# Kernel optimization log

Measured on AMD Instinct MI355X. Metric: run time of the kernel, lower is better.

Reference implementation:

```python
import jax, jax.numpy as jnp
import numpy as np

D = 128
H = 4
DK = D // H


def _spmm(row, col, val, x, n):
    # sparse.mm(adj, x) with adj in COO form: out[row] += val * x[col]
    return jax.ops.segment_sum(val[:, None] * x[col], row, num_segments=n)


def _arrg(h, a1_w, a1_b, a2_w, a2_b):
    return jax.nn.leaky_relu(h @ a1_w + a1_b, negative_slope=0.01) @ a2_w + a2_b


def _cross_attn(x, q_x, q_w, k_w, v_w):
    n, d = x.shape
    m = q_x.shape[0]
    q = (q_x @ q_w).reshape(m, H, DK).transpose(1, 0, 2)   # [H, Q, dk]
    k = (x @ k_w).reshape(n, H, DK).transpose(1, 0, 2)     # [H, N, dk]
    v = (q_x @ v_w).reshape(m, H, DK).transpose(1, 0, 2)   # [H, Q, dk]
    s = jnp.einsum('hnd,hqd->hnq', k, q) / jnp.sqrt(jnp.float32(DK))
    w = jax.nn.softmax(s, axis=-1)                          # softmax over queries
    out = jnp.einsum('hnq,hqd->hnd', w, v).transpose(1, 0, 2).reshape(n, d)
    return out + x


def setup_inputs() -> dict:
    key = jax.random.key(0)
    ks = iter(jax.random.split(key, 64))
    nrm = lambda shape, s=0.05: jax.random.normal(next(ks), shape, jnp.float32) * s
    inp = {}
    inp['trans_w'] = nrm((1, D)); inp['trans_b'] = nrm((D,))
    inp['g_w'] = nrm((D, D));     inp['g_b'] = nrm((D,))
    inp['qg_w'] = nrm((D, D));    inp['qg_b'] = nrm((D,))
    inp['q_w'] = nrm((D, D)); inp['k_w'] = nrm((D, D)); inp['v_w'] = nrm((D, D))
    inp['a1_w'] = nrm((D, 2 * D)); inp['a1_b'] = nrm((2 * D,))
    inp['a2_w'] = nrm((2 * D, D)); inp['a2_b'] = nrm((D,))
    inp['x0'] = jax.random.normal(next(ks), (25000,), jnp.float32)
    inp['q0'] = jax.random.normal(next(ks), (100,), jnp.float32)
    for i in (1, 2, 3):
        inp[f'xin{i}'] = jax.random.normal(next(ks), (25000,), jnp.float32)
        inp[f'qin{i}'] = jax.random.normal(next(ks), (100,), jnp.float32)
    n_sizes = {1: 50000, 2: 75000, 3: 100000}
    q_sizes = {1: 200, 2: 300, 3: 400}
    for i in (1, 2, 3):
        e = 16 * n_sizes[i]
        inp[f'aval{i}'] = jax.random.uniform(next(ks), (e,), jnp.float32)
        inp[f'arow{i}'] = jax.random.randint(next(ks), (e,), 0, n_sizes[i], jnp.int64)
        inp[f'acol{i}'] = jax.random.randint(next(ks), (e,), 0, n_sizes[i], jnp.int64)
        qe = 16 * q_sizes[i]
        inp[f'qval{i}'] = jax.random.uniform(next(ks), (qe,), jnp.float32)
        inp[f'qrow{i}'] = jax.random.randint(next(ks), (qe,), 0, q_sizes[i], jnp.int64)
        inp[f'qcol{i}'] = jax.random.randint(next(ks), (qe,), 0, q_sizes[i], jnp.int64)
    return inp


def reference(trans_w, trans_b, g_w, g_b, qg_w, qg_b, q_w, k_w, v_w,
              a1_w, a1_b, a2_w, a2_b,
              x0, q0, xin1, xin2, xin3, qin1, qin2, qin3,
              aval1, aval2, aval3, qval1, qval2, qval3,
              arow1, acol1, arow2, acol2, arow3, acol3,
              qrow1, qcol1, qrow2, qcol2, qrow3, qcol3):
    trans = lambda v: v[:, None] @ trans_w + trans_b
    x = trans(x0)
    qx = trans(q0)
    steps = [
        (xin1, qin1, arow1, acol1, aval1, qrow1, qcol1, qval1, 50000, 200),
        (xin2, qin2, arow2, acol2, aval2, qrow2, qcol2, qval2, 75000, 300),
        (xin3, qin3, arow3, acol3, aval3, qrow3, qcol3, qval3, 100000, 400),
    ]
    for xin, qin, ar, ac, av, qr, qc, qv, n, m in steps:
        x = jnp.concatenate([x, trans(xin)], axis=0)
        qx = jnp.concatenate([qx, trans(qin)], axis=0)
        x = _spmm(ar, ac, av, x @ g_w + g_b, n)
        qx = _spmm(qr, qc, qv, qx @ qg_w + qg_b, m)
        x = _arrg(x, a1_w, a1_b, a2_w, a2_b)
        qx = _arrg(qx, a1_w, a1_b, a2_w, a2_b)
        x = _cross_attn(x, qx, q_w, k_w, v_w)
    return (x, qx)
```

## Files before the change

kernel.cpp:

```cpp
#include <hip/hip_runtime.h>

typedef unsigned short u16;
typedef __attribute__((ext_vector_type(8))) short bf16x8;
typedef __attribute__((ext_vector_type(4))) float f32x4;
typedef __attribute__((ext_vector_type(2))) unsigned u32x2;

__device__ __forceinline__ float b2f(u16 v) {
    return __uint_as_float(((unsigned)v) << 16);
}
__device__ __forceinline__ u16 f2b(float x) {
    unsigned u = __float_as_uint(x);
    unsigned r = u + 0x7FFFu + ((u >> 16) & 1u);
    return (u16)(r >> 16);
}
__device__ __forceinline__ float4 load_bf4(const u16* p) {
    ushort4 q = *(const ushort4*)p;
    float4 f;
    f.x = b2f(q.x); f.y = b2f(q.y); f.z = b2f(q.z); f.w = b2f(q.w);
    return f;
}
__device__ __forceinline__ float4 in4(const void* p, long off, bool bf) {
    if (bf) return load_bf4((const u16*)p + off);
    return *(const float4*)((const float*)p + off);
}
// ... 45 lines not shown
                                 const void* __restrict__ k_w, const void* __restrict__ q_w,
                                 const void* __restrict__ v_w,
                                 u16* __restrict__ Wg, u16* __restrict__ Wqg,
                                 u16* __restrict__ Wa1, u16* __restrict__ Wa2,
                                 u16* __restrict__ Wk, u16* __restrict__ Wq,
                                 u16* __restrict__ Wv, const int* __restrict__ flags) {
    const bool bf = flags[0] != 0;
    int idx = blockIdx.x * blockDim.x + threadIdx.x;
    const void* src; u16* dst; int K, N, loc;
    if (idx < 32768) {
        if (idx < 16384) { src = g_w; dst = Wg; loc = idx; }
        else { src = qg_w; dst = Wqg; loc = idx - 16384; }
        K = 128; N = 128;
    } else if (idx < 65536) { src = a1_w; dst = Wa1; loc = idx - 32768; K = 128; N = 256; }
    else if (idx < 98304)  { src = a2_w; dst = Wa2; loc = idx - 65536; K = 256; N = 128; }
    else if (idx < 147456) {
        if (idx < 114688) { src = k_w; dst = Wk; loc = idx - 98304; }
        else if (idx < 131072) { src = q_w; dst = Wq; loc = idx - 114688; }
        else { src = v_w; dst = Wv; loc = idx - 131072; }
        K = 128; N = 128;
    } else return;
    int j = loc & 7, lane = (loc >> 3) & 63, t = loc >> 9;
    int KC = K >> 5;
    int kc = t % KC, ct = t / KC;
    int k = kc * 32 + (lane >> 4) * 8 + j;
    int nn = ct * 16 + (lane & 15);
    dst[loc] = f2b(in1(src, (long)k * N + nn, bf));
}

template<int KTOT, int NOUT, bool LEAKY, typename AT, typename CT>
__launch_bounds__(256)
__global__ void gemm_mfma_kernel(const AT* __restrict__ A, const u16* __restrict__ Wf,
                                 const void* __restrict__ bias, CT* __restrict__ C,
                                 int n, const int* __restrict__ flags) {
    constexpr int KC = KTOT / 32;
    constexpr int NT = NOUT / 16;
    __shared__ u16 wlds[KTOT * NOUT];
    {
        const int4* srcw = (const int4*)Wf;
        int4* dstw = (int4*)wlds;
        constexpr int NV = KTOT * NOUT * 2 / 16;
#pragma unroll
        for (int i = 0; i < NV / 256; ++i)
            dstw[i * 256 + threadIdx.x] = srcw[i * 256 + threadIdx.x];
    }
    __syncthreads();
    const bool bf = flags[0] != 0;
    const int lane = threadIdx.x & 63;
    const int wave = threadIdx.x >> 6;
    const int quad = lane >> 4, col = lane & 15;
    const int rbase = (blockIdx.x * 4 + wave) * 16;
    if (rbase >= n) return;
    int node = rbase + col; if (node >= n) node = n - 1;
    f32x4 acc[NT];
#pragma unroll
    for (int ct = 0; ct < NT; ++ct) acc[ct] = (f32x4){0.f, 0.f, 0.f, 0.f};
#pragma unroll
    for (int kc = 0; kc < KC; ++kc) {
        bf16x8 af;
        if constexpr (sizeof(AT) == 2) {
            af = *(const bf16x8*)((const u16*)A + (size_t)node * KTOT + kc * 32 + quad * 8);
        } else {
            const float* ap = (const float*)A + (size_t)node * KTOT + kc * 32 + quad * 8;
            float4 a0 = *(const float4*)ap;
            float4 a1 = *(const float4*)(ap + 4);
            af[0] = (short)f2b(a0.x); af[1] = (short)f2b(a0.y);
            af[2] = (short)f2b(a0.z); af[3] = (short)f2b(a0.w);
            af[4] = (short)f2b(a1.x); af[5] = (short)f2b(a1.y);
            af[6] = (short)f2b(a1.z); af[7] = (short)f2b(a1.w);
        }
#pragma unroll
        for (int ct = 0; ct < NT; ++ct) {
            bf16x8 wf = *(const bf16x8*)(wlds + (((ct * KC + kc) * 64 + lane) * 8));
            acc[ct] = __builtin_amdgcn_mfma_f32_16x16x32_bf16(af, wf, acc[ct], 0, 0, 0);
        }
    }
#pragma unroll
    for (int ct = 0; ct < NT; ++ct) {
        int colg = ct * 16 + col;
        float b = bias ? in1(bias, colg, bf) : 0.f;
#pragma unroll
        for (int r = 0; r < 4; ++r) {
            int row = rbase + quad * 4 + r;
            if (row >= n) continue;
            float v = acc[ct][r] + b;
            if (LEAKY) v = v > 0.f ? v : 0.01f * v;
            if constexpr (sizeof(CT) == 2) C[(size_t)row * NOUT + colg] = (CT)f2b(v);
            else                           C[(size_t)row * NOUT + colg] = (CT)v;
        }
    }
}

__launch_bounds__(256)
__global__ void gemm_qv_kernel(const float* __restrict__ A, const u16* __restrict__ Wfq,
                               const u16* __restrict__ Wfv, u16* __restrict__ Qf,
                               u16* __restrict__ Vf, int m, int mt32) {
    __shared__ u16 wldsq[128 * 128];
    __shared__ u16 wldsv[128 * 128];
    {
        const int4* sq = (const int4*)Wfq;
        const int4* sv = (const int4*)Wfv;
        int4* dq = (int4*)wldsq;
        int4* dv = (int4*)wldsv;
#pragma unroll
        for (int i = 0; i < 8; ++i) {
            dq[i * 256 + threadIdx.x] = sq[i * 256 + threadIdx.x];
            dv[i * 256 + threadIdx.x] = sv[i * 256 + threadIdx.x];
        }
    }
    __syncthreads();
    const int mpad = mt32 * 32;
    const int mt16 = mt32 * 2;
    const int lane = threadIdx.x & 63;
    const int wave = threadIdx.x >> 6;
    const int quad = lane >> 4, col = lane & 15;
    const int rbase = (blockIdx.x * 4 + wave) * 16;
    if (rbase >= mpad) return;
    int node = rbase + col; if (node >= m) node = m - 1;
    f32x4 accq[8], accv[8];
#pragma unroll
    for (int ct = 0; ct < 8; ++ct) {
        accq[ct] = (f32x4){0.f, 0.f, 0.f, 0.f};
        accv[ct] = (f32x4){0.f, 0.f, 0.f, 0.f};
    }
#pragma unroll
    for (int kc = 0; kc < 4; ++kc) {
        const float* ap = A + (size_t)node * 128 + kc * 32 + quad * 8;
        float4 a0 = *(const float4*)ap;
        float4 a1 = *(const float4*)(ap + 4);
        bf16x8 af;
        af[0] = (short)f2b(a0.x); af[1] = (short)f2b(a0.y);
        af[2] = (short)f2b(a0.z); af[3] = (short)f2b(a0.w);
        af[4] = (short)f2b(a1.x); af[5] = (short)f2b(a1.y);
        af[6] = (short)f2b(a1.z); af[7] = (short)f2b(a1.w);
#pragma unroll
        for (int ct = 0; ct < 8; ++ct) {
            bf16x8 wq = *(const bf16x8*)(wldsq + (((ct * 4 + kc) * 64 + lane) * 8));
            bf16x8 wv = *(const bf16x8*)(wldsv + (((ct * 4 + kc) * 64 + lane) * 8));
            accq[ct] = __builtin_amdgcn_mfma_f32_16x16x32_bf16(af, wq, accq[ct], 0, 0, 0);
            accv[ct] = __builtin_amdgcn_mfma_f32_16x16x32_bf16(af, wv, accv[ct], 0, 0, 0);
        }
    }
    const float qscale = 0.17677669529663687f * 1.44269504088896340736f;
#pragma unroll
    for (int ct = 0; ct < 8; ++ct) {
        int colg = ct * 16 + col;
        int h = colg >> 5, dim = colg & 31;
#pragma unroll
        for (int r = 0; r < 4; ++r) {
            int row = rbase + quad * 4 + r;
            if (row >= mpad) continue;
            bool pad = row >= m;
            float vq = pad ? 0.f : accq[ct][r] * qscale;
            float vv = pad ? 0.f : accv[ct][r];
            {
                size_t idx = ((((size_t)h * mt16 + (row >> 4)) * 64)
                              + ((dim >> 3) << 4) + (row & 15)) * 8 + (dim & 7);
                Qf[idx] = f2b(vq);
            }
            {
                size_t idx = (((((size_t)h * mt32 + (row >> 5)) * 2 + (dim >> 4)) * 64)
                              + (((row >> 3) & 3) << 4) + (dim & 15)) * 8 + (row & 7);
                Vf[idx] = f2b(vv);
            }
        }
    }
}

#define RSH 8
#define NBC_MAX 512
#define EPB 4096
#define BSTRIDE 6144

__global__ void ginit_kernel(int* __restrict__ p, int nbc) {
    int i = blockIdx.x * blockDim.x + threadIdx.x;
    if (i < nbc) p[i] = i * BSTRIDE;
}

__launch_bounds__(256)
__global__ void qbuild_kernel(const void* __restrict__ rows, const void* __restrict__ colsin,
                              const void* __restrict__ valsin, int e, int nrows,
                              int2* __restrict__ pack1, int* __restrict__ rowptr,
                              int* __restrict__ rowend, const int* __restrict__ flags) {
    __shared__ int hist[512], cur[512], sc[512];
    const bool bf = flags[0] != 0;
    const bool i64 = flags[1] != 0;
    const int tid = threadIdx.x;
    for (int i = tid; i < 512; i += 256) hist[i] = 0;
    __syncthreads();
    for (int i = tid; i < e; i += 256)
        atomicAdd(&hist[inIdx(rows, i, i64)], 1);
    __syncthreads();
    int v0 = hist[tid], v1 = hist[tid + 256];
    sc[tid] = v0; sc[tid + 256] = v1;
    __syncthreads();
    for (int off = 1; off < 512; off <<= 1) {
        int a = (tid >= off) ? sc[tid - off] : 0;
        int b = sc[tid + 256 - off];
        __syncthreads();
        sc[tid] += a;
        sc[tid + 256] += b;
        __syncthreads();
    }
    {
        int x = sc[tid] - v0;
        cur[tid] = x;
        if (tid < nrows) { rowptr[tid] = x; rowend[tid] = x + v0; }
        int x1 = sc[tid + 256] - v1;
        cur[tid + 256] = x1;
        if (tid + 256 < nrows) { rowptr[tid + 256] = x1; rowend[tid + 256] = x1 + v1; }
    }
    __syncthreads();
    for (int i = tid; i < e; i += 256) {
        int r = inIdx(rows, i, i64);
        int p = atomicAdd(&cur[r], 1);
        pack1[p] = (int2){inIdx(colsin, i, i64), __float_as_int(in1(valsin, i, bf))};
    }
}

__launch_bounds__(256)
__global__ void psort_kernel(const void* __restrict__ rows, const void* __restrict__ colsin,
                             const void* __restrict__ valsin, int e,
                             int* __restrict__ gcur, int2* __restrict__ pack0,
                             int nbc, const int* __restrict__ flags) {
    __shared__ int hist[NBC_MAX];
    __shared__ int scan[NBC_MAX];
    __shared__ int base[NBC_MAX];
    __shared__ int cur[NBC_MAX];
    __shared__ int2 stage[EPB];
    __shared__ u16 binof[EPB];
    const bool bf = flags[0] != 0;
    const bool i64 = flags[1] != 0;
    const int tid = threadIdx.x;
    const long s0 = (long)blockIdx.x * EPB;
    int cnt_e = e - (int)s0; if (cnt_e > EPB) cnt_e = EPB;

    for (int i = tid; i < NBC_MAX; i += 256) hist[i] = 0;
    __syncthreads();
    for (int j = tid; j < cnt_e; j += 256)
        atomicAdd(&hist[inIdx(rows, s0 + j, i64) >> RSH], 1);
    __syncthreads();
    for (int i = tid; i < NBC_MAX; i += 256) scan[i] = hist[i];
    __syncthreads();
    for (int off = 1; off < NBC_MAX; off <<= 1) {
        int a = (tid >= off) ? scan[tid - off] : 0;
        int c = scan[tid + 256 - off];
        __syncthreads();
        scan[tid] += a;
        scan[tid + 256] += c;
        __syncthreads();
    }
    for (int i = tid; i < nbc; i += 256) {
        int h = hist[i];
        cur[i] = scan[i] - h;
        base[i] = h ? atomicAdd(&gcur[i], h) : 0;
    }
    __syncthreads();
    for (int j = tid; j < cnt_e; j += 256) {
        int r = inIdx(rows, s0 + j, i64);
        int bin = r >> RSH;
        int p = atomicAdd(&cur[bin], 1);
        int2 pk;
        pk.x = ((r & ((1 << RSH) - 1)) << 20) | inIdx(colsin, s0 + j, i64);
        pk.y = __float_as_int(in1(valsin, s0 + j, bf));
        stage[p] = pk;
        binof[p] = (u16)bin;
    }
    __syncthreads();
    for (int j = tid; j < cnt_e; j += 256) {
        int bin = binof[j];
        int st = scan[bin] - hist[bin];
        pack0[base[bin] + (j - st)] = stage[j];
    }
}

__launch_bounds__(256)
__global__ void breorder256_kernel(const int2* __restrict__ pack0, const int* __restrict__ bend,
                                   int2* __restrict__ pack1,
                                   int* __restrict__ rowptr, int* __restrict__ rowend, int n) {
    __shared__ int hist[256], scan[256], cur[256];
    const int b = blockIdx.x;
    const int s = b * BSTRIDE, e = bend[b];
    const int tid = threadIdx.x;
    hist[tid] = 0;
    __syncthreads();
    for (int i = s + tid; i < e; i += 256)
        atomicAdd(&hist[(unsigned)pack0[i].x >> 20], 1);
    __syncthreads();
    scan[tid] = hist[tid];
    __syncthreads();
    for (int off = 1; off < 256; off <<= 1) {
        int a = (tid >= off) ? scan[tid - off] : 0;
        __syncthreads();
        scan[tid] += a;
        __syncthreads();
    }
    int st = s + scan[tid] - hist[tid];
    cur[tid] = st;
    int rg = (b << RSH) + tid;
    if (rg < n) { rowptr[rg] = st; rowend[rg] = st + hist[tid]; }
    __syncthreads();
    for (int i = s + tid; i < e; i += 256) {
        int2 pk = pack0[i];
        int rl = (unsigned)pk.x >> 20;
        int p = atomicAdd(&cur[rl], 1);
        pack1[p] = (int2){pk.x & 0xFFFFF, pk.y};
    }
}

__device__ __forceinline__ void bffma8(float v, uint4 h, float* a) {
    a[0] += v * __uint_as_float(h.x << 16);
    a[1] += v * __uint_as_float(h.x & 0xFFFF0000u);
    a[2] += v * __uint_as_float(h.y << 16);
    a[3] += v * __uint_as_float(h.y & 0xFFFF0000u);
    a[4] += v * __uint_as_float(h.z << 16);
    a[5] += v * __uint_as_float(h.z & 0xFFFF0000u);
    a[6] += v * __uint_as_float(h.w << 16);
    a[7] += v * __uint_as_float(h.w & 0xFFFF0000u);
// ... 8 lines not shown
    const int s16 = lane >> 4;
    const int l16 = lane & 15;
    int s = rowptr[r], e = rowend[r];
    float a[8] = {0.f, 0.f, 0.f, 0.f, 0.f, 0.f, 0.f, 0.f};
    int i = s + s16;
    for (; i + 12 < e; i += 16) {
        int2 p0 = pack[i], p1 = pack[i + 4], p2 = pack[i + 8], p3 = pack[i + 12];
        uint4 h0 = *(const uint4*)(H + (size_t)p0.x * 128 + l16 * 8);
        uint4 h1 = *(const uint4*)(H + (size_t)p1.x * 128 + l16 * 8);
        uint4 h2 = *(const uint4*)(H + (size_t)p2.x * 128 + l16 * 8);
        uint4 h3 = *(const uint4*)(H + (size_t)p3.x * 128 + l16 * 8);
        bffma8(__int_as_float(p0.y), h0, a);
        bffma8(__int_as_float(p1.y), h1, a);
        bffma8(__int_as_float(p2.y), h2, a);
        bffma8(__int_as_float(p3.y), h3, a);
    }
    for (; i < e; i += 4) {
        int2 p0 = pack[i];
        uint4 h0 = *(const uint4*)(H + (size_t)p0.x * 128 + l16 * 8);
        bffma8(__int_as_float(p0.y), h0, a);
    }
#pragma unroll
    for (int k = 0; k < 8; ++k) {
        a[k] += __shfl_xor(a[k], 16, 64);
        a[k] += __shfl_xor(a[k], 32, 64);
    }
    if (s16 == 0) {
        uint4 o;
        o.x = (unsigned)f2b(a[0]) | ((unsigned)f2b(a[1]) << 16);
        o.y = (unsigned)f2b(a[2]) | ((unsigned)f2b(a[3]) << 16);
        o.z = (unsigned)f2b(a[4]) | ((unsigned)f2b(a[5]) << 16);
        o.w = (unsigned)f2b(a[6]) | ((unsigned)f2b(a[7]) << 16);
        *(uint4*)(out + (size_t)r * 128 + l16 * 8) = o;
    }
}

__launch_bounds__(256)
__global__ void attn_mfma_kernel(const u16* __restrict__ Kb, const u16* __restrict__ Qf,
                                 const u16* __restrict__ Vf, float* __restrict__ X,
                                 int n, int m, int mt32, int pad) {
    __shared__ __align__(128) u16 Pbuf_all[4 * 1024];
    const int h = blockIdx.y;
    const int wave = threadIdx.x >> 6;
    const int lane = threadIdx.x & 63;
    const int nb = (blockIdx.x * 4 + wave) * 32;
    if (nb >= n) return;
    const int quad = lane >> 4, col = lane & 15;
    int node0 = nb + col;      if (node0 >= n) node0 = n - 1;
    int node1 = nb + 16 + col; if (node1 >= n) node1 = n - 1;
    bf16x8 kf0 = *(const bf16x8*)(Kb + (size_t)node0 * 128 + h * 32 + quad * 8);
    bf16x8 kf1 = *(const bf16x8*)(Kb + (size_t)node1 * 128 + h * 32 + quad * 8);
    f32x4 O00 = {0.f, 0.f, 0.f, 0.f}, O01 = {0.f, 0.f, 0.f, 0.f};
    f32x4 O10 = {0.f, 0.f, 0.f, 0.f}, O11 = {0.f, 0.f, 0.f, 0.f};
    const f32x4 zero = {0.f, 0.f, 0.f, 0.f};
    float Lp0[4] = {0.f, 0.f, 0.f, 0.f};
    float Lp1[4] = {0.f, 0.f, 0.f, 0.f};
    u16* Pw0 = Pbuf_all + wave * 1024;
    u16* Pw1 = Pw0 + 512;
    uint2* pw0[2]; uint2* pw1[2];
    pw0[0] = (uint2*)(Pw0 + col * 16 + quad * 4);
    pw0[1] = (uint2*)(Pw0 + 256 + col * 16 + quad * 4);
    pw1[0] = (uint2*)(Pw1 + col * 16 + quad * 4);
    pw1[1] = (uint2*)(Pw1 + 256 + col * 16 + quad * 4);
    const unsigned paddr0 = (unsigned)(uintptr_t)Pw0 + (unsigned)(quad * 256 + col * 8);
    const unsigned paddr1 = (unsigned)(uintptr_t)Pw1 + (unsigned)(quad * 256 + col * 8);
    const u16* Qbase = Qf + (size_t)h * (mt32 * 2) * 512;
// ... 134 lines not shown
    };
    int*   flags = (int*)alloc(256);
    const int NMAX = 100000;
    const int NBINS = (NMAX + 255) >> RSH;
    float* X   = (float*)alloc((size_t)NMAX * 128 * 4);
    u16*   T1b = (u16*)  alloc((size_t)NMAX * 128 * 2);
    u16*   Xs  = (u16*)  alloc((size_t)NMAX * 128 * 2);
    u16*   T2  = (u16*)  alloc((size_t)NMAX * 256 * 2);
    float* QX  = (float*)alloc((size_t)400 * 128 * 4);
    u16*   QT1b= (u16*)  alloc((size_t)400 * 128 * 2);
    u16*   QXs = (u16*)  alloc((size_t)400 * 128 * 2);
    u16*   QT2 = (u16*)  alloc((size_t)400 * 256 * 2);
    u16*   Qfrag = (u16*)alloc((size_t)4 * 13 * 1024 * 2);
    u16*   Vfrag = (u16*)alloc((size_t)4 * 13 * 1024 * 2);
    u16* Wg  = (u16*)alloc((size_t)128 * 128 * 2);
    u16* Wqg = (u16*)alloc((size_t)128 * 128 * 2);
    u16* Wa1 = (u16*)alloc((size_t)128 * 256 * 2);
    u16* Wa2 = (u16*)alloc((size_t)256 * 128 * 2);
    u16* Wk  = (u16*)alloc((size_t)128 * 128 * 2);
    u16* Wq  = (u16*)alloc((size_t)128 * 128 * 2);
    u16* Wv  = (u16*)alloc((size_t)128 * 128 * 2);
    int2*  csr_pack = (int2*)alloc((size_t)(NBINS + 1) * BSTRIDE * 8);
    int*   bktcur = (int*)alloc((size_t)NBC_MAX * 4);
    int*   rowptr = (int*)alloc((size_t)NMAX * 4);
    int*   rowend = (int*)alloc((size_t)NMAX * 4);
    int2*  pack0  = (int2*)T2;

    sniff_kernel<<<1, 64, 0, stream>>>((const u16*)x0, (const int*)d_in[iarow[0]], flags);

    wprep_all_kernel<<<(147456 + 255) / 256, 256, 0, stream>>>(
        g_w, qg_w, a1_w, a2_w, k_w, q_w, v_w,
        Wg, Wqg, Wa1, Wa2, Wk, Wq, Wv, flags);

    auto launch_trans2 = [&](const void* vx, float* outx, int rowsx,
                             const void* vq, float* outq, int rowsq) {
        int tot = (rowsx + rowsq) * 32;
        trans2_kernel<<<(tot + 255) / 256, 256, 0, stream>>>(vx, outx, rowsx,
                                                             vq, outq, rowsq,
                                                             trans_w, trans_b, flags);
    };
    auto build_spmm = [&](const void* rows, const void* colsidx, const void* vals, int e,
                          int nrows, const u16* H, u16* OUT) {
        if (nrows <= 512) {
            qbuild_kernel<<<1, 256, 0, stream>>>(rows, colsidx, vals, e, nrows,
                                                 csr_pack, rowptr, rowend, flags);
        } else {
            int nbc = (nrows + 255) >> RSH;
            ginit_kernel<<<(nbc + 255) / 256, 256, 0, stream>>>(bktcur, nbc);
            psort_kernel<<<(e + EPB - 1) / EPB, 256, 0, stream>>>(rows, colsidx, vals, e,
                                                                  bktcur, pack0, nbc, flags);
            breorder256_kernel<<<nbc, 256, 0, stream>>>(pack0, bktcur, csr_pack,
                                                        rowptr, rowend, nrows);
        }
        spmm_kernel<<<(nrows + 3) / 4, 256, 0, stream>>>(H, rowptr, rowend, csr_pack,
                                                         OUT, nrows);
    };

    int nprev = in_sizes[13];
    int mprev = in_sizes[14];
    launch_trans2(x0, X, nprev, q0, QX, mprev);

    const int ns[3] = {50000, 75000, 100000};
    const int ms[3] = {200, 300, 400};
    for (int s = 0; s < 3; ++s) {
        const int n = ns[s], m = ms[s];
        const int e  = in_sizes[iaval[s]];
        const int qe = in_sizes[iqval[s]];
        launch_trans2(d_in[ixin[s]], X + (size_t)nprev * 128, n - nprev,
                      d_in[iqin[s]], QX + (size_t)mprev * 128, m - mprev);
        const int gb  = (n + 63) / 64;
        const int gqb = (m + 63) / 64;
        gemm_mfma_kernel<128, 128, false, float, u16><<<gb, 256, 0, stream>>>(X, Wg, g_b, T1b, n, flags);
        build_spmm(d_in[iarow[s]], d_in[iacol[s]], d_in[iaval[s]], e, n, T1b, Xs);
        gemm_mfma_kernel<128, 128, false, float, u16><<<gqb, 256, 0, stream>>>(QX, Wqg, qg_b, QT1b, m, flags);
        build_spmm(d_in[iqrow[s]], d_in[iqcol[s]], d_in[iqval[s]], qe, m, QT1b, QXs);
        gemm_mfma_kernel<128, 256, true, u16, u16><<<gb, 256, 0, stream>>>(Xs, Wa1, a1_b, T2, n, flags);
        gemm_mfma_kernel<256, 128, false, u16, float><<<gb, 256, 0, stream>>>(T2, Wa2, a2_b, X, n, flags);
        gemm_mfma_kernel<128, 256, true, u16, u16><<<gqb, 256, 0, stream>>>(QXs, Wa1, a1_b, QT2, m, flags);
        gemm_mfma_kernel<256, 128, false, u16, float><<<gqb, 256, 0, stream>>>(QT2, Wa2, a2_b, QX, m, flags);
        const int mt32 = (m + 31) / 32;
        const int pad = mt32 * 32 - m;
        gemm_mfma_kernel<128, 128, false, float, u16><<<gb, 256, 0, stream>>>(X, Wk, nullptr, T1b, n, flags);
        gemm_qv_kernel<<<(mt32 * 32 + 63) / 64, 256, 0, stream>>>(QX, Wq, Wv, Qfrag, Vfrag, m, mt32);
        attn_mfma_kernel<<<dim3((n + 127) / 128, 4), 256, 0, stream>>>(T1b, Qfrag, Vfrag, X, n, m, mt32, pad);
        nprev = n;
        mprev = m;
    }

    const int n4t = (100000 + 400) * 128 / 4;
    out_writer_kernel<<<(n4t + 255) / 256, 256, 0, stream>>>(X, QX, d_out, flags);
}
```

Measured before the change: 1.144 ms.

## Fuse query-branch pipeline into one kernel and fold trans into the g-GEMM

The whole small query-side step (trans, qg GEMM, CSR build, SpMM, two MLP GEMMs, Q/V projection) is merged into a single 1024-thread block kernel that reloads weights into shared memory between phases. The per-step trans kernel for new x rows is folded into the A-load of the first GEMM, and the bucket cursor reset moves into breorder. These changes cut kernel launch count and avoid materialising the new trans rows. The cost is that the query work now runs serially on one CU with many block-wide barriers, and csr_pack is shared between the query and node paths, which relies on stream ordering.

```diff
diff --git a/kernel.cpp b/kernel.cpp
--- a/kernel.cpp
+++ b/kernel.cpp
@@ -101,7 +101,9 @@
 __launch_bounds__(256)
 __global__ void gemm_mfma_kernel(const AT* __restrict__ A, const u16* __restrict__ Wf,
                                  const void* __restrict__ bias, CT* __restrict__ C,
-                                 int n, const int* __restrict__ flags) {
+                                 int n, const int* __restrict__ flags,
+                                 const void* __restrict__ vap, int nprevP,
+                                 const void* __restrict__ twp, const void* __restrict__ tbp) {
     constexpr int KC = KTOT / 32;
     constexpr int NT = NOUT / 16;
     __shared__ u16 wlds[KTOT * NOUT];
@@ -130,13 +132,24 @@
         if constexpr (sizeof(AT) == 2) {
             af = *(const bf16x8*)((const u16*)A + (size_t)node * KTOT + kc * 32 + quad * 8);
         } else {
-            const float* ap = (const float*)A + (size_t)node * KTOT + kc * 32 + quad * 8;
-            float4 a0 = *(const float4*)ap;
-            float4 a1 = *(const float4*)(ap + 4);
-            af[0] = (short)f2b(a0.x); af[1] = (short)f2b(a0.y);
-            af[2] = (short)f2b(a0.z); af[3] = (short)f2b(a0.w);
-            af[4] = (short)f2b(a1.x); af[5] = (short)f2b(a1.y);
-            af[6] = (short)f2b(a1.z); af[7] = (short)f2b(a1.w);
+            int c0 = kc * 32 + quad * 8;
+            if (vap && node >= nprevP) {
+                float v = in1(vap, node - nprevP, bf);
+                float4 w0 = in4(twp, c0, bf), w1 = in4(twp, c0 + 4, bf);
+                float4 b0 = in4(tbp, c0, bf), b1 = in4(tbp, c0 + 4, bf);
+                af[0] = (short)f2b(v * w0.x + b0.x); af[1] = (short)f2b(v * w0.y + b0.y);
+                af[2] = (short)f2b(v * w0.z + b0.z); af[3] = (short)f2b(v * w0.w + b0.w);
+                af[4] = (short)f2b(v * w1.x + b1.x); af[5] = (short)f2b(v * w1.y + b1.y);
+                af[6] = (short)f2b(v * w1.z + b1.z); af[7] = (short)f2b(v * w1.w + b1.w);
+            } else {
+                const float* ap = (const float*)A + (size_t)node * KTOT + c0;
+                float4 a0 = *(const float4*)ap;
+                float4 a1 = *(const float4*)(ap + 4);
+                af[0] = (short)f2b(a0.x); af[1] = (short)f2b(a0.y);
+                af[2] = (short)f2b(a0.z); af[3] = (short)f2b(a0.w);
+                af[4] = (short)f2b(a1.x); af[5] = (short)f2b(a1.y);
+                af[6] = (short)f2b(a1.z); af[7] = (short)f2b(a1.w);
+            }
         }
 #pragma unroll
         for (int ct = 0; ct < NT; ++ct) {
@@ -160,82 +173,6 @@
     }
 }
 
-__launch_bounds__(256)
-__global__ void gemm_qv_kernel(const float* __restrict__ A, const u16* __restrict__ Wfq,
-                               const u16* __restrict__ Wfv, u16* __restrict__ Qf,
-                               u16* __restrict__ Vf, int m, int mt32) {
-    __shared__ u16 wldsq[128 * 128];
-    __shared__ u16 wldsv[128 * 128];
-    {
-        const int4* sq = (const int4*)Wfq;
-        const int4* sv = (const int4*)Wfv;
-        int4* dq = (int4*)wldsq;
-        int4* dv = (int4*)wldsv;
-#pragma unroll
-        for (int i = 0; i < 8; ++i) {
-            dq[i * 256 + threadIdx.x] = sq[i * 256 + threadIdx.x];
-            dv[i * 256 + threadIdx.x] = sv[i * 256 + threadIdx.x];
-        }
-    }
-    __syncthreads();
-    const int mpad = mt32 * 32;
-    const int mt16 = mt32 * 2;
-    const int lane = threadIdx.x & 63;
-    const int wave = threadIdx.x >> 6;
-    const int quad = lane >> 4, col = lane & 15;
-    const int rbase = (blockIdx.x * 4 + wave) * 16;
-    if (rbase >= mpad) return;
-    int node = rbase + col; if (node >= m) node = m - 1;
-    f32x4 accq[8], accv[8];
-#pragma unroll
-    for (int ct = 0; ct < 8; ++ct) {
-        accq[ct] = (f32x4){0.f, 0.f, 0.f, 0.f};
-        accv[ct] = (f32x4){0.f, 0.f, 0.f, 0.f};
-    }
-#pragma unroll
-    for (int kc = 0; kc < 4; ++kc) {
-        const float* ap = A + (size_t)node * 128 + kc * 32 + quad * 8;
-        float4 a0 = *(const float4*)ap;
-        float4 a1 = *(const float4*)(ap + 4);
-        bf16x8 af;
-        af[0] = (short)f2b(a0.x); af[1] = (short)f2b(a0.y);
-        af[2] = (short)f2b(a0.z); af[3] = (short)f2b(a0.w);
-        af[4] = (short)f2b(a1.x); af[5] = (short)f2b(a1.y);
-        af[6] = (short)f2b(a1.z); af[7] = (short)f2b(a1.w);
-#pragma unroll
-        for (int ct = 0; ct < 8; ++ct) {
-            bf16x8 wq = *(const bf16x8*)(wldsq + (((ct * 4 + kc) * 64 + lane) * 8));
-            bf16x8 wv = *(const bf16x8*)(wldsv + (((ct * 4 + kc) * 64 + lane) * 8));
-            accq[ct] = __builtin_amdgcn_mfma_f32_16x16x32_bf16(af, wq, accq[ct], 0, 0, 0);
-            accv[ct] = __builtin_amdgcn_mfma_f32_16x16x32_bf16(af, wv, accv[ct], 0, 0, 0);
-        }
-    }
-    const float qscale = 0.17677669529663687f * 1.44269504088896340736f;
-#pragma unroll
-    for (int ct = 0; ct < 8; ++ct) {
-        int colg = ct * 16 + col;
-        int h = colg >> 5, dim = colg & 31;
-#pragma unroll
-        for (int r = 0; r < 4; ++r) {
-            int row = rbase + quad * 4 + r;
-            if (row >= mpad) continue;
-            bool pad = row >= m;
-            float vq = pad ? 0.f : accq[ct][r] * qscale;
-            float vv = pad ? 0.f : accv[ct][r];
-            {
-                size_t idx = ((((size_t)h * mt16 + (row >> 4)) * 64)
-                              + ((dim >> 3) << 4) + (row & 15)) * 8 + (dim & 7);
-                Qf[idx] = f2b(vq);
-            }
-            {
-                size_t idx = (((((size_t)h * mt32 + (row >> 5)) * 2 + (dim >> 4)) * 64)
-                              + (((row >> 3) & 3) << 4) + (dim & 15)) * 8 + (row & 7);
-                Vf[idx] = f2b(vv);
-            }
-        }
-    }
-}
-
 #define RSH 8
 #define NBC_MAX 512
 #define EPB 4096
@@ -244,47 +181,6 @@
 __global__ void ginit_kernel(int* __restrict__ p, int nbc) {
     int i = blockIdx.x * blockDim.x + threadIdx.x;
     if (i < nbc) p[i] = i * BSTRIDE;
-}
-
-__launch_bounds__(256)
-__global__ void qbuild_kernel(const void* __restrict__ rows, const void* __restrict__ colsin,
-                              const void* __restrict__ valsin, int e, int nrows,
-                              int2* __restrict__ pack1, int* __restrict__ rowptr,
-                              int* __restrict__ rowend, const int* __restrict__ flags) {
-    __shared__ int hist[512], cur[512], sc[512];
-    const bool bf = flags[0] != 0;
-    const bool i64 = flags[1] != 0;
-    const int tid = threadIdx.x;
-    for (int i = tid; i < 512; i += 256) hist[i] = 0;
-    __syncthreads();
-    for (int i = tid; i < e; i += 256)
-        atomicAdd(&hist[inIdx(rows, i, i64)], 1);
-    __syncthreads();
-    int v0 = hist[tid], v1 = hist[tid + 256];
-    sc[tid] = v0; sc[tid + 256] = v1;
-    __syncthreads();
-    for (int off = 1; off < 512; off <<= 1) {
-        int a = (tid >= off) ? sc[tid - off] : 0;
-        int b = sc[tid + 256 - off];
-        __syncthreads();
-        sc[tid] += a;
-        sc[tid + 256] += b;
-        __syncthreads();
-    }
-    {
-        int x = sc[tid] - v0;
-        cur[tid] = x;
-        if (tid < nrows) { rowptr[tid] = x; rowend[tid] = x + v0; }
-        int x1 = sc[tid + 256] - v1;
-        cur[tid + 256] = x1;
-        if (tid + 256 < nrows) { rowptr[tid + 256] = x1; rowend[tid + 256] = x1 + v1; }
-    }
-    __syncthreads();
-    for (int i = tid; i < e; i += 256) {
-        int r = inIdx(rows, i, i64);
-        int p = atomicAdd(&cur[r], 1);
-        pack1[p] = (int2){inIdx(colsin, i, i64), __float_as_int(in1(valsin, i, bf))};
-    }
 }
 
 __launch_bounds__(256)
@@ -344,7 +240,7 @@
 }
 
 __launch_bounds__(256)
-__global__ void breorder256_kernel(const int2* __restrict__ pack0, const int* __restrict__ bend,
+__global__ void breorder256_kernel(const int2* __restrict__ pack0, int* __restrict__ bend,
                                    int2* __restrict__ pack1,
                                    int* __restrict__ rowptr, int* __restrict__ rowend, int n) {
     __shared__ int hist[256], scan[256], cur[256];
@@ -353,6 +249,7 @@
     const int tid = threadIdx.x;
     hist[tid] = 0;
     __syncthreads();
+    if (tid == 0) bend[b] = b * BSTRIDE;
     for (int i = s + tid; i < e; i += 256)
         atomicAdd(&hist[(unsigned)pack0[i].x >> 20], 1);
     __syncthreads();
@@ -427,6 +324,282 @@
         o.z = (unsigned)f2b(a[4]) | ((unsigned)f2b(a[5]) << 16);
         o.w = (unsigned)f2b(a[6]) | ((unsigned)f2b(a[7]) << 16);
         *(uint4*)(out + (size_t)r * 128 + l16 * 8) = o;
+    }
+}
+
+__launch_bounds__(1024)
+__global__ void qstep_kernel(float* __restrict__ QX, const void* __restrict__ qin, int mprev,
+                             const u16* __restrict__ Wqg, const void* __restrict__ qg_b,
+                             const u16* __restrict__ Wa1, const void* __restrict__ a1_b,
+                             const u16* __restrict__ Wa2, const void* __restrict__ a2_b,
+                             const u16* __restrict__ Wq, const u16* __restrict__ Wv,
+                             const void* __restrict__ qrow, const void* __restrict__ qcol,
+                             const void* __restrict__ qval, int qe,
+                             u16* __restrict__ QT1b, u16* __restrict__ QXs,
+                             u16* __restrict__ QT2,
+                             int2* __restrict__ qpack,
+                             u16* __restrict__ Qf, u16* __restrict__ Vf,
+                             int m, int mt32,
+                             const void* __restrict__ tw, const void* __restrict__ tb,
+                             const int* __restrict__ flags) {
+    __shared__ u16 wbuf[32768];
+    __shared__ int hist[512], cur[512], sc[512];
+    const bool bf = flags[0] != 0;
+    const bool i64 = flags[1] != 0;
+    const int tid = threadIdx.x;
+    const int lane = tid & 63;
+    const int wv = tid >> 6;
+    const int quad = lane >> 4, col = lane & 15;
+    const int ntile = (m + 15) >> 4;
+    const f32x4 zero4 = {0.f, 0.f, 0.f, 0.f};
+
+    {
+        const int4* s4 = (const int4*)Wqg;
+        int4* d4 = (int4*)wbuf;
+        for (int i = tid; i < 2048; i += 1024) d4[i] = s4[i];
+    }
+    __syncthreads();
+    for (int t = wv; t < ntile; t += 16) {
+        int rbase = t * 16;
+        int node = rbase + col; if (node >= m) node = m - 1;
+        f32x4 acc[8];
+#pragma unroll
+        for (int ct = 0; ct < 8; ++ct) acc[ct] = zero4;
+#pragma unroll
+        for (int kc = 0; kc < 4; ++kc) {
+            bf16x8 af;
+            int c0 = kc * 32 + quad * 8;
+            if (node >= mprev) {
+                float v = in1(qin, node - mprev, bf);
+                float4 w0 = in4(tw, c0, bf), w1 = in4(tw, c0 + 4, bf);
+                float4 b0 = in4(tb, c0, bf), b1 = in4(tb, c0 + 4, bf);
+                af[0] = (short)f2b(v * w0.x + b0.x); af[1] = (short)f2b(v * w0.y + b0.y);
+                af[2] = (short)f2b(v * w0.z + b0.z); af[3] = (short)f2b(v * w0.w + b0.w);
+                af[4] = (short)f2b(v * w1.x + b1.x); af[5] = (short)f2b(v * w1.y + b1.y);
+                af[6] = (short)f2b(v * w1.z + b1.z); af[7] = (short)f2b(v * w1.w + b1.w);
+            } else {
+                const float* ap = QX + (size_t)node * 128 + c0;
+                float4 a0 = *(const float4*)ap, a1 = *(const float4*)(ap + 4);
+                af[0] = (short)f2b(a0.x); af[1] = (short)f2b(a0.y);
+                af[2] = (short)f2b(a0.z); af[3] = (short)f2b(a0.w);
+                af[4] = (short)f2b(a1.x); af[5] = (short)f2b(a1.y);
+                af[6] = (short)f2b(a1.z); af[7] = (short)f2b(a1.w);
+            }
+#pragma unroll
+            for (int ct = 0; ct < 8; ++ct) {
+                bf16x8 wf = *(const bf16x8*)(wbuf + (((ct * 4 + kc) * 64 + lane) * 8));
+                acc[ct] = __builtin_amdgcn_mfma_f32_16x16x32_bf16(af, wf, acc[ct], 0, 0, 0);
+            }
+        }
+#pragma unroll
+        for (int ct = 0; ct < 8; ++ct) {
+            int colg = ct * 16 + col;
+            float b = in1(qg_b, colg, bf);
+#pragma unroll
+            for (int r = 0; r < 4; ++r) {
+                int row = rbase + quad * 4 + r;
+                if (row < m) QT1b[(size_t)row * 128 + colg] = f2b(acc[ct][r] + b);
+            }
+        }
+    }
+    for (int i = tid; i < 512; i += 1024) hist[i] = 0;
+    __syncthreads();
+    for (int i = tid; i < qe; i += 1024)
+        atomicAdd(&hist[inIdx(qrow, i, i64)], 1);
+    __syncthreads();
+    int v0 = (tid < 512) ? hist[tid] : 0;
+    if (tid < 512) sc[tid] = v0;
+    __syncthreads();
+    for (int off = 1; off < 512; off <<= 1) {
+        int a = (tid < 512 && tid >= off) ? sc[tid - off] : 0;
+        __syncthreads();
+        if (tid < 512) sc[tid] += a;
+        __syncthreads();
+    }
+    if (tid < 512) {
+        int x = sc[tid] - v0;
+        hist[tid] = x;
+        cur[tid] = x;
+    }
+    __syncthreads();
+    for (int i = tid; i < qe; i += 1024) {
+        int r = inIdx(qrow, i, i64);
+        int p = atomicAdd(&cur[r], 1);
+        qpack[p] = (int2){inIdx(qcol, i, i64), __float_as_int(in1(qval, i, bf))};
+    }
+    __syncthreads();
+    __threadfence();
+    {
+        const int s16 = lane >> 4, l16 = lane & 15;
+        for (int r = wv; r < m; r += 16) {
+            int s = hist[r], e = sc[r];
+            float a[8] = {0.f, 0.f, 0.f, 0.f, 0.f, 0.f, 0.f, 0.f};
+            int i = s + s16;
+            for (; i + 12 < e; i += 16) {
+                int2 p0 = qpack[i], p1 = qpack[i + 4], p2 = qpack[i + 8], p3 = qpack[i + 12];
+                uint4 h0 = *(const uint4*)(QT1b + (size_t)p0.x * 128 + l16 * 8);
+                uint4 h1 = *(const uint4*)(QT1b + (size_t)p1.x * 128 + l16 * 8);
+                uint4 h2 = *(const uint4*)(QT1b + (size_t)p2.x * 128 + l16 * 8);
+                uint4 h3 = *(const uint4*)(QT1b + (size_t)p3.x * 128 + l16 * 8);
+                bffma8(__int_as_float(p0.y), h0, a);
+                bffma8(__int_as_float(p1.y), h1, a);
+                bffma8(__int_as_float(p2.y), h2, a);
+                bffma8(__int_as_float(p3.y), h3, a);
+            }
+            for (; i < e; i += 4) {
+                int2 p0 = qpack[i];
+                uint4 h0 = *(const uint4*)(QT1b + (size_t)p0.x * 128 + l16 * 8);
+                bffma8(__int_as_float(p0.y), h0, a);
+            }
+#pragma unroll
+            for (int k = 0; k < 8; ++k) {
+                a[k] += __shfl_xor(a[k], 16, 64);
+                a[k] += __shfl_xor(a[k], 32, 64);
+            }
+            if (s16 == 0) {
+                uint4 o;
+                o.x = (unsigned)f2b(a[0]) | ((unsigned)f2b(a[1]) << 16);
+                o.y = (unsigned)f2b(a[2]) | ((unsigned)f2b(a[3]) << 16);
+                o.z = (unsigned)f2b(a[4]) | ((unsigned)f2b(a[5]) << 16);
+                o.w = (unsigned)f2b(a[6]) | ((unsigned)f2b(a[7]) << 16);
+                *(uint4*)(QXs + (size_t)r * 128 + l16 * 8) = o;
+            }
+        }
+    }
+    __syncthreads();
+    __threadfence();
+    {
+        const int4* s4 = (const int4*)Wa1;
+        int4* d4 = (int4*)wbuf;
+        for (int i = tid; i < 4096; i += 1024) d4[i] = s4[i];
+    }
+    __syncthreads();
+    for (int t = wv; t < ntile; t += 16) {
+        int rbase = t * 16;
+        int node = rbase + col; if (node >= m) node = m - 1;
+        f32x4 acc[16];
+#pragma unroll
+        for (int ct = 0; ct < 16; ++ct) acc[ct] = zero4;
+#pragma unroll
+        for (int kc = 0; kc < 4; ++kc) {
+            bf16x8 af = *(const bf16x8*)(QXs + (size_t)node * 128 + kc * 32 + quad * 8);
+#pragma unroll
+            for (int ct = 0; ct < 16; ++ct) {
+                bf16x8 wf = *(const bf16x8*)(wbuf + (((ct * 4 + kc) * 64 + lane) * 8));
+                acc[ct] = __builtin_amdgcn_mfma_f32_16x16x32_bf16(af, wf, acc[ct], 0, 0, 0);
+            }
+        }
+#pragma unroll
+        for (int ct = 0; ct < 16; ++ct) {
+            int colg = ct * 16 + col;
+            float b = in1(a1_b, colg, bf);
+#pragma unroll
+            for (int r = 0; r < 4; ++r) {
+                int row = rbase + quad * 4 + r;
+                if (row < m) {
+                    float v = acc[ct][r] + b;
+                    v = v > 0.f ? v : 0.01f * v;
+                    QT2[(size_t)row * 256 + colg] = f2b(v);
+                }
+            }
+        }
+    }
+    __syncthreads();
+    __threadfence();
+    {
+        const int4* s4 = (const int4*)Wa2;
+        int4* d4 = (int4*)wbuf;
+        for (int i = tid; i < 4096; i += 1024) d4[i] = s4[i];
+    }
+    __syncthreads();
+    for (int t = wv; t < ntile; t += 16) {
+        int rbase = t * 16;
+        int node = rbase + col; if (node >= m) node = m - 1;
+        f32x4 acc[8];
+#pragma unroll
+        for (int ct = 0; ct < 8; ++ct) acc[ct] = zero4;
+#pragma unroll
+        for (int kc = 0; kc < 8; ++kc) {
+            bf16x8 af = *(const bf16x8*)(QT2 + (size_t)node * 256 + kc * 32 + quad * 8);
+#pragma unroll
+            for (int ct = 0; ct < 8; ++ct) {
+                bf16x8 wf = *(const bf16x8*)(wbuf + (((ct * 8 + kc) * 64 + lane) * 8));
+                acc[ct] = __builtin_amdgcn_mfma_f32_16x16x32_bf16(af, wf, acc[ct], 0, 0, 0);
+            }
+        }
+#pragma unroll
+        for (int ct = 0; ct < 8; ++ct) {
+            int colg = ct * 16 + col;
+            float b = in1(a2_b, colg, bf);
+#pragma unroll
+            for (int r = 0; r < 4; ++r) {
+                int row = rbase + quad * 4 + r;
+                if (row < m) QX[(size_t)row * 128 + colg] = acc[ct][r] + b;
+            }
+        }
+    }
+    __syncthreads();
+    __threadfence();
+    {
+        const int4* s4q = (const int4*)Wq;
+        const int4* s4v = (const int4*)Wv;
+        int4* d4 = (int4*)wbuf;
+        for (int i = tid; i < 2048; i += 1024) {
+            d4[i] = s4q[i];
+            d4[2048 + i] = s4v[i];
+        }
+    }
+    __syncthreads();
+    const int mpad = mt32 * 32;
+    const int mt16 = mt32 * 2;
+    const int ntileF = mt16;
+    const float qscale = 0.17677669529663687f * 1.44269504088896340736f;
+    for (int t = wv; t < ntileF; t += 16) {
+        int rbase = t * 16;
+        int node = rbase + col; if (node >= m) node = m - 1;
+        f32x4 accq[8], accv[8];
+#pragma unroll
+        for (int ct = 0; ct < 8; ++ct) { accq[ct] = zero4; accv[ct] = zero4; }
+#pragma unroll
+        for (int kc = 0; kc < 4; ++kc) {
+            const float* ap = QX + (size_t)node * 128 + kc * 32 + quad * 8;
+            float4 a0 = *(const float4*)ap, a1 = *(const float4*)(ap + 4);
+            bf16x8 af;
+            af[0] = (short)f2b(a0.x); af[1] = (short)f2b(a0.y);
+            af[2] = (short)f2b(a0.z); af[3] = (short)f2b(a0.w);
+            af[4] = (short)f2b(a1.x); af[5] = (short)f2b(a1.y);
+            af[6] = (short)f2b(a1.z); af[7] = (short)f2b(a1.w);
+#pragma unroll
+            for (int ct = 0; ct < 8; ++ct) {
+                bf16x8 wq = *(const bf16x8*)(wbuf + (((ct * 4 + kc) * 64 + lane) * 8));
+                bf16x8 wvv = *(const bf16x8*)(wbuf + 16384 + (((ct * 4 + kc) * 64 + lane) * 8));
+                accq[ct] = __builtin_amdgcn_mfma_f32_16x16x32_bf16(af, wq, accq[ct], 0, 0, 0);
+                accv[ct] = __builtin_amdgcn_mfma_f32_16x16x32_bf16(af, wvv, accv[ct], 0, 0, 0);
+            }
+        }
+#pragma unroll
+        for (int ct = 0; ct < 8; ++ct) {
+            int colg = ct * 16 + col;
+            int h = colg >> 5, dim = colg & 31;
+#pragma unroll
+            for (int r = 0; r < 4; ++r) {
+                int row = rbase + quad * 4 + r;
+                if (row >= mpad) continue;
+                bool pad = row >= m;
+                float vq = pad ? 0.f : accq[ct][r] * qscale;
+                float vv = pad ? 0.f : accv[ct][r];
+                {
+                    size_t idx = ((((size_t)h * mt16 + (row >> 4)) * 64)
+                                  + ((dim >> 3) << 4) + (row & 15)) * 8 + (dim & 7);
+                    Qf[idx] = f2b(vq);
+                }
+                {
+                    size_t idx = (((((size_t)h * mt32 + (row >> 5)) * 2 + (dim >> 4)) * 64)
+                                  + (((row >> 3) & 3) << 4) + (dim & 15)) * 8 + (row & 7);
+                    Vf[idx] = f2b(vv);
+                }
+            }
+        }
     }
 }
 
@@ -627,33 +800,14 @@
         g_w, qg_w, a1_w, a2_w, k_w, q_w, v_w,
         Wg, Wqg, Wa1, Wa2, Wk, Wq, Wv, flags);
 
-    auto launch_trans2 = [&](const void* vx, float* outx, int rowsx,
-                             const void* vq, float* outq, int rowsq) {
-        int tot = (rowsx + rowsq) * 32;
-        trans2_kernel<<<(tot + 255) / 256, 256, 0, stream>>>(vx, outx, rowsx,
-                                                             vq, outq, rowsq,
-                                                             trans_w, trans_b, flags);
-    };
-    auto build_spmm = [&](const void* rows, const void* colsidx, const void* vals, int e,
-                          int nrows, const u16* H, u16* OUT) {
-        if (nrows <= 512) {
-            qbuild_kernel<<<1, 256, 0, stream>>>(rows, colsidx, vals, e, nrows,
-                                                 csr_pack, rowptr, rowend, flags);
-        } else {
-            int nbc = (nrows + 255) >> RSH;
-            ginit_kernel<<<(nbc + 255) / 256, 256, 0, stream>>>(bktcur, nbc);
-            psort_kernel<<<(e + EPB - 1) / EPB, 256, 0, stream>>>(rows, colsidx, vals, e,
-                                                                  bktcur, pack0, nbc, flags);
-            breorder256_kernel<<<nbc, 256, 0, stream>>>(pack0, bktcur, csr_pack,
-                                                        rowptr, rowend, nrows);
-        }
-        spmm_kernel<<<(nrows + 3) / 4, 256, 0, stream>>>(H, rowptr, rowend, csr_pack,
-                                                         OUT, nrows);
-    };
-
     int nprev = in_sizes[13];
     int mprev = in_sizes[14];
-    launch_trans2(x0, X, nprev, q0, QX, mprev);
+    {
+        int tot = (nprev + mprev) * 32;
+        trans2_kernel<<<(tot + 255) / 256, 256, 0, stream>>>(x0, X, nprev, q0, QX, mprev,
+                                                             trans_w, trans_b, flags);
+    }
+    ginit_kernel<<<(NBC_MAX + 255) / 256, 256, 0, stream>>>(bktcur, NBC_MAX);
 
     const int ns[3] = {50000, 75000, 100000};
     const int ms[3] = {200, 300, 400};
@@ -661,23 +815,32 @@
         const int n = ns[s], m = ms[s];
         const int e  = in_sizes[iaval[s]];
         const int qe = in_sizes[iqval[s]];
-        launch_trans2(d_in[ixin[s]], X + (size_t)nprev * 128, n - nprev,
-                      d_in[iqin[s]], QX + (size_t)mprev * 128, m - mprev);
         const int gb  = (n + 63) / 64;
-        const int gqb = (m + 63) / 64;
-        gemm_mfma_kernel<128, 128, false, float, u16><<<gb, 256, 0, stream>>>(X, Wg, g_b, T1b, n, flags);
-        build_spmm(d_in[iarow[s]], d_in[iacol[s]], d_in[iaval[s]], e, n, T1b, Xs);
-        gemm_mfma_kernel<128, 128, false, float, u16><<<gqb, 256, 0, stream>>>(QX, Wqg, qg_b, QT1b, m, flags);
-        build_spmm(d_in[iqrow[s]], d_in[iqcol[s]], d_in[iqval[s]], qe, m, QT1b, QXs);
-        gemm_mfma_kernel<128, 256, true, u16, u16><<<gb, 256, 0, stream>>>(Xs, Wa1, a1_b, T2, n, flags);
-        gemm_mfma_kernel<256, 128, false, u16, float><<<gb, 256, 0, stream>>>(T2, Wa2, a2_b, X, n, flags);
-        gemm_mfma_kernel<128, 256, true, u16, u16><<<gqb, 256, 0, stream>>>(QXs, Wa1, a1_b, QT2, m, flags);
-        gemm_mfma_kernel<256, 128, false, u16, float><<<gqb, 256, 0, stream>>>(QT2, Wa2, a2_b, QX, m, flags);
         const int mt32 = (m + 31) / 32;
         const int pad = mt32 * 32 - m;
-        gemm_mfma_kernel<128, 128, false, float, u16><<<gb, 256, 0, stream>>>(X, Wk, nullptr, T1b, n, flags);
-        gemm_qv_kernel<<<(mt32 * 32 + 63) / 64, 256, 0, stream>>>(QX, Wq, Wv, Qfrag, Vfrag, m, mt32);
-        attn_mfma_kernel<<<dim3((n + 127) / 128, 4), 256, 0, stream>>>(T1b, Qfrag, Vfrag, X, n, m, mt32, pad);
+        gemm_mfma_kernel<128, 128, false, float, u16><<<gb, 256, 0, stream>>>(
+            X, Wg, g_b, T1b, n, flags, d_in[ixin[s]], nprev, trans_w, trans_b);
+        {
+            int nbc = (n + 255) >> RSH;
+            psort_kernel<<<(e + EPB - 1) / EPB, 256, 0, stream>>>(
+                d_in[iarow[s]], d_in[iacol[s]], d_in[iaval[s]], e, bktcur, pack0, nbc, flags);
+            breorder256_kernel<<<nbc, 256, 0, stream>>>(pack0, bktcur, csr_pack,
+                                                        rowptr, rowend, n);
+            spmm_kernel<<<(n + 3) / 4, 256, 0, stream>>>(T1b, rowptr, rowend, csr_pack,
+                                                         Xs, n);
+        }
+        qstep_kernel<<<1, 1024, 0, stream>>>(
+            QX, d_in[iqin[s]], mprev, Wqg, qg_b, Wa1, a1_b, Wa2, a2_b, Wq, Wv,
+            d_in[iqrow[s]], d_in[iqcol[s]], d_in[iqval[s]], qe,
+            QT1b, QXs, QT2, csr_pack, Qfrag, Vfrag, m, mt32, trans_w, trans_b, flags);
+        gemm_mfma_kernel<128, 256, true, u16, u16><<<gb, 256, 0, stream>>>(
+            Xs, Wa1, a1_b, T2, n, flags, nullptr, 0, nullptr, nullptr);
+        gemm_mfma_kernel<256, 128, false, u16, float><<<gb, 256, 0, stream>>>(
+            T2, Wa2, a2_b, X, n, flags, nullptr, 0, nullptr, nullptr);
+        gemm_mfma_kernel<128, 128, false, float, u16><<<gb, 256, 0, stream>>>(
+            X, Wk, nullptr, T1b, n, flags, nullptr, 0, nullptr, nullptr);
+        attn_mfma_kernel<<<dim3((n + 127) / 128, 4), 256, 0, stream>>>(
+            T1b, Qfrag, Vfrag, X, n, m, mt32, pad);
         nprev = n;
         mprev = m;
     }
```

Result: slower. 1.925 ms (+68.3%).

## Fuse per-step trans into gemm A-load and self-reset bucket cursors

Applied to the files above, without the earlier changes.

The per-step trans2 launch is removed. The g/qg GEMM now computes the trans (v*w+b) on the fly for newly appended rows instead of reading them from X. The bucket cursor reset (ginit) is hoisted to a single launch up front, with breorder resetting its own bucket's cursor after use, which drops one launch per step. The fused path adds a branch in the GEMM A-load, and the new rows are never written to X. Later stages overwrite X anyway, so this looks safe.

```diff
diff --git a/kernel.cpp b/kernel.cpp
--- a/kernel.cpp
+++ b/kernel.cpp
@@ -101,7 +101,9 @@
 __launch_bounds__(256)
 __global__ void gemm_mfma_kernel(const AT* __restrict__ A, const u16* __restrict__ Wf,
                                  const void* __restrict__ bias, CT* __restrict__ C,
-                                 int n, const int* __restrict__ flags) {
+                                 int n, const int* __restrict__ flags,
+                                 const void* __restrict__ vap, int nprevP,
+                                 const void* __restrict__ twp, const void* __restrict__ tbp) {
     constexpr int KC = KTOT / 32;
     constexpr int NT = NOUT / 16;
     __shared__ u16 wlds[KTOT * NOUT];
@@ -130,13 +132,24 @@
         if constexpr (sizeof(AT) == 2) {
             af = *(const bf16x8*)((const u16*)A + (size_t)node * KTOT + kc * 32 + quad * 8);
         } else {
-            const float* ap = (const float*)A + (size_t)node * KTOT + kc * 32 + quad * 8;
-            float4 a0 = *(const float4*)ap;
-            float4 a1 = *(const float4*)(ap + 4);
-            af[0] = (short)f2b(a0.x); af[1] = (short)f2b(a0.y);
-            af[2] = (short)f2b(a0.z); af[3] = (short)f2b(a0.w);
-            af[4] = (short)f2b(a1.x); af[5] = (short)f2b(a1.y);
-            af[6] = (short)f2b(a1.z); af[7] = (short)f2b(a1.w);
+            int c0 = kc * 32 + quad * 8;
+            if (vap && node >= nprevP) {
+                float v = in1(vap, node - nprevP, bf);
+                float4 w0 = in4(twp, c0, bf), w1 = in4(twp, c0 + 4, bf);
+                float4 b0 = in4(tbp, c0, bf), b1 = in4(tbp, c0 + 4, bf);
+                af[0] = (short)f2b(v * w0.x + b0.x); af[1] = (short)f2b(v * w0.y + b0.y);
+                af[2] = (short)f2b(v * w0.z + b0.z); af[3] = (short)f2b(v * w0.w + b0.w);
+                af[4] = (short)f2b(v * w1.x + b1.x); af[5] = (short)f2b(v * w1.y + b1.y);
+                af[6] = (short)f2b(v * w1.z + b1.z); af[7] = (short)f2b(v * w1.w + b1.w);
+            } else {
+                const float* ap = (const float*)A + (size_t)node * KTOT + c0;
+                float4 a0 = *(const float4*)ap;
+                float4 a1 = *(const float4*)(ap + 4);
+                af[0] = (short)f2b(a0.x); af[1] = (short)f2b(a0.y);
+                af[2] = (short)f2b(a0.z); af[3] = (short)f2b(a0.w);
+                af[4] = (short)f2b(a1.x); af[5] = (short)f2b(a1.y);
+                af[6] = (short)f2b(a1.z); af[7] = (short)f2b(a1.w);
+            }
         }
 #pragma unroll
         for (int ct = 0; ct < NT; ++ct) {
@@ -344,7 +357,7 @@
 }
 
 __launch_bounds__(256)
-__global__ void breorder256_kernel(const int2* __restrict__ pack0, const int* __restrict__ bend,
+__global__ void breorder256_kernel(const int2* __restrict__ pack0, int* __restrict__ bend,
                                    int2* __restrict__ pack1,
                                    int* __restrict__ rowptr, int* __restrict__ rowend, int n) {
     __shared__ int hist[256], scan[256], cur[256];
@@ -353,6 +366,7 @@
     const int tid = threadIdx.x;
     hist[tid] = 0;
     __syncthreads();
+    if (tid == 0) bend[b] = b * BSTRIDE;
     for (int i = s + tid; i < e; i += 256)
         atomicAdd(&hist[(unsigned)pack0[i].x >> 20], 1);
     __syncthreads();
@@ -627,33 +641,14 @@
         g_w, qg_w, a1_w, a2_w, k_w, q_w, v_w,
         Wg, Wqg, Wa1, Wa2, Wk, Wq, Wv, flags);
 
-    auto launch_trans2 = [&](const void* vx, float* outx, int rowsx,
-                             const void* vq, float* outq, int rowsq) {
-        int tot = (rowsx + rowsq) * 32;
-        trans2_kernel<<<(tot + 255) / 256, 256, 0, stream>>>(vx, outx, rowsx,
-                                                             vq, outq, rowsq,
-                                                             trans_w, trans_b, flags);
-    };
-    auto build_spmm = [&](const void* rows, const void* colsidx, const void* vals, int e,
-                          int nrows, const u16* H, u16* OUT) {
-        if (nrows <= 512) {
-            qbuild_kernel<<<1, 256, 0, stream>>>(rows, colsidx, vals, e, nrows,
-                                                 csr_pack, rowptr, rowend, flags);
-        } else {
-            int nbc = (nrows + 255) >> RSH;
-            ginit_kernel<<<(nbc + 255) / 256, 256, 0, stream>>>(bktcur, nbc);
-            psort_kernel<<<(e + EPB - 1) / EPB, 256, 0, stream>>>(rows, colsidx, vals, e,
-                                                                  bktcur, pack0, nbc, flags);
-            breorder256_kernel<<<nbc, 256, 0, stream>>>(pack0, bktcur, csr_pack,
-                                                        rowptr, rowend, nrows);
-        }
-        spmm_kernel<<<(nrows + 3) / 4, 256, 0, stream>>>(H, rowptr, rowend, csr_pack,
-                                                         OUT, nrows);
-    };
-
     int nprev = in_sizes[13];
     int mprev = in_sizes[14];
-    launch_trans2(x0, X, nprev, q0, QX, mprev);
+    {
+        int tot = (nprev + mprev) * 32;
+        trans2_kernel<<<(tot + 255) / 256, 256, 0, stream>>>(x0, X, nprev, q0, QX, mprev,
+                                                             trans_w, trans_b, flags);
+    }
+    ginit_kernel<<<(NBC_MAX + 255) / 256, 256, 0, stream>>>(bktcur, NBC_MAX);
 
     const int ns[3] = {50000, 75000, 100000};
     const int ms[3] = {200, 300, 400};
@@ -661,23 +656,40 @@
         const int n = ns[s], m = ms[s];
         const int e  = in_sizes[iaval[s]];
         const int qe = in_sizes[iqval[s]];
-        launch_trans2(d_in[ixin[s]], X + (size_t)nprev * 128, n - nprev,
-                      d_in[iqin[s]], QX + (size_t)mprev * 128, m - mprev);
         const int gb  = (n + 63) / 64;
         const int gqb = (m + 63) / 64;
-        gemm_mfma_kernel<128, 128, false, float, u16><<<gb, 256, 0, stream>>>(X, Wg, g_b, T1b, n, flags);
-        build_spmm(d_in[iarow[s]], d_in[iacol[s]], d_in[iaval[s]], e, n, T1b, Xs);
-        gemm_mfma_kernel<128, 128, false, float, u16><<<gqb, 256, 0, stream>>>(QX, Wqg, qg_b, QT1b, m, flags);
-        build_spmm(d_in[iqrow[s]], d_in[iqcol[s]], d_in[iqval[s]], qe, m, QT1b, QXs);
-        gemm_mfma_kernel<128, 256, true, u16, u16><<<gb, 256, 0, stream>>>(Xs, Wa1, a1_b, T2, n, flags);
-        gemm_mfma_kernel<256, 128, false, u16, float><<<gb, 256, 0, stream>>>(T2, Wa2, a2_b, X, n, flags);
-        gemm_mfma_kernel<128, 256, true, u16, u16><<<gqb, 256, 0, stream>>>(QXs, Wa1, a1_b, QT2, m, flags);
-        gemm_mfma_kernel<256, 128, false, u16, float><<<gqb, 256, 0, stream>>>(QT2, Wa2, a2_b, QX, m, flags);
         const int mt32 = (m + 31) / 32;
         const int pad = mt32 * 32 - m;
-        gemm_mfma_kernel<128, 128, false, float, u16><<<gb, 256, 0, stream>>>(X, Wk, nullptr, T1b, n, flags);
+        gemm_mfma_kernel<128, 128, false, float, u16><<<gb, 256, 0, stream>>>(
+            X, Wg, g_b, T1b, n, flags, d_in[ixin[s]], nprev, trans_w, trans_b);
+        {
+            int nbc = (n + 255) >> RSH;
+            psort_kernel<<<(e + EPB - 1) / EPB, 256, 0, stream>>>(
+                d_in[iarow[s]], d_in[iacol[s]], d_in[iaval[s]], e, bktcur, pack0, nbc, flags);
+            breorder256_kernel<<<nbc, 256, 0, stream>>>(pack0, bktcur, csr_pack,
+                                                        rowptr, rowend, n);
+            spmm_kernel<<<(n + 3) / 4, 256, 0, stream>>>(T1b, rowptr, rowend, csr_pack,
+                                                         Xs, n);
+        }
+        gemm_mfma_kernel<128, 128, false, float, u16><<<gqb, 256, 0, stream>>>(
+            QX, Wqg, qg_b, QT1b, m, flags, d_in[iqin[s]], mprev, trans_w, trans_b);
+        qbuild_kernel<<<1, 256, 0, stream>>>(d_in[iqrow[s]], d_in[iqcol[s]], d_in[iqval[s]],
+                                             qe, m, csr_pack, rowptr, rowend, flags);
+        spmm_kernel<<<(m + 3) / 4, 256, 0, stream>>>(QT1b, rowptr, rowend, csr_pack,
+                                                     QXs, m);
+        gemm_mfma_kernel<128, 256, true, u16, u16><<<gb, 256, 0, stream>>>(
+            Xs, Wa1, a1_b, T2, n, flags, nullptr, 0, nullptr, nullptr);
+        gemm_mfma_kernel<256, 128, false, u16, float><<<gb, 256, 0, stream>>>(
+            T2, Wa2, a2_b, X, n, flags, nullptr, 0, nullptr, nullptr);
+        gemm_mfma_kernel<128, 256, true, u16, u16><<<gqb, 256, 0, stream>>>(
+            QXs, Wa1, a1_b, QT2, m, flags, nullptr, 0, nullptr, nullptr);
+        gemm_mfma_kernel<256, 128, false, u16, float><<<gqb, 256, 0, stream>>>(
+            QT2, Wa2, a2_b, QX, m, flags, nullptr, 0, nullptr, nullptr);
+        gemm_mfma_kernel<128, 128, false, float, u16><<<gb, 256, 0, stream>>>(
+            X, Wk, nullptr, T1b, n, flags, nullptr, 0, nullptr, nullptr);
         gemm_qv_kernel<<<(mt32 * 32 + 63) / 64, 256, 0, stream>>>(QX, Wq, Wv, Qfrag, Vfrag, m, mt32);
-        attn_mfma_kernel<<<dim3((n + 127) / 128, 4), 256, 0, stream>>>(T1b, Qfrag, Vfrag, X, n, m, mt32, pad);
+        attn_mfma_kernel<<<dim3((n + 127) / 128, 4), 256, 0, stream>>>(
+            T1b, Qfrag, Vfrag, X, n, m, mt32, pad);
         nprev = n;
         mprev = m;
     }
```

Result: no change. 1.126 ms (-1.6%).
